# Optimization experiments

Hardware: AMD Instinct MI355X
Metric: run time of the kernel (lower is better)

The kernel has to match this reference:

```python
import jax, jax.numpy as jnp
import numpy as np

B, L, D = 8, 8192, 512


def setup_inputs() -> dict:
    key = jax.random.key(0)
    ks = jax.random.split(key, 8)
    sc = 1.0 / np.sqrt(D).astype(np.float32)
    return {
        "emotion_h": jax.random.normal(ks[0], (B, 1, D), jnp.float32),
        "sents_h": jax.random.normal(ks[1], (B, L, D), jnp.float32),
        "pre_sents_h": jax.random.normal(ks[2], (B, L, D), jnp.float32),
        "pos_sents_h": jax.random.normal(ks[3], (B, L, D), jnp.float32),
        "W1": jax.random.normal(ks[4], (D, D), jnp.float32) * sc,
        "b1": jnp.zeros((D,), jnp.float32),
        "W2": jax.random.normal(ks[5], (D, D), jnp.float32) * sc,
        "b2": jnp.zeros((D,), jnp.float32),
        "W3": jax.random.normal(ks[6], (D, 1), jnp.float32) * sc,
        "b3": jnp.zeros((1,), jnp.float32),
    }


def reference(emotion_h, sents_h, pre_sents_h, pos_sents_h, W1, b1, W2, b2, W3, b3):
    # Attention: score over sentences conditioned on emotion vector.
    eq = emotion_h @ W1 + b1                      # (B, 1, D)
    sq = sents_h @ W2 + b2                        # (B, L, D)
    logits = (jnp.tanh(eq + sq) @ W3 + b3)[..., 0]  # (B, L)
    s = jax.nn.softmax(logits, axis=-1)           # (B, L), sums to 1 over L

    # Original builds (B,L,3,L) tril/eye/triu masks and matmuls with the
    # expanded score -> per-position weights are:
    #   pre_w[i]  = sum_{j<i} s[j]   (tril(-1))
    #   self_w[i] = s[i]             (eye)
    #   pos_w[i]  = sum_{j>i} s[j]   (triu(+1))
    # Equivalent O(L) form via cumsum:
    c = jnp.cumsum(s, axis=-1)                    # inclusive prefix sum
    pre_w = (c - s)[..., None]                    # exclusive prefix sum
    self_w = s[..., None]
    pos_w = (1.0 - c)[..., None]                  # suffix sum (softmax sums to 1)

    # Weighted combine of the three contexts: sum over the 3-context axis.
    return pre_w * pre_sents_h + self_w * sents_h + pos_w * pos_sents_h
```

## Files before the change

kernel.cpp:

```cpp
#include <hip/hip_runtime.h>
#include <hip/hip_bf16.h>

typedef __bf16 v8bf __attribute__((ext_vector_type(8)));
typedef float  v4f  __attribute__((ext_vector_type(4)));

__device__ __forceinline__ float fast_tanh(float x) {
    x = fminf(fmaxf(x, -15.f), 15.f);
    float t = __builtin_amdgcn_exp2f(x * 2.885390081777927f);
    return (t - 1.f) * __builtin_amdgcn_rcpf(t + 1.f);
}

__device__ __forceinline__ v8bf cvt8(float4 f0, float4 f1) {
    v8bf v;
    v[0] = (__bf16)f0.x; v[1] = (__bf16)f0.y; v[2] = (__bf16)f0.z; v[3] = (__bf16)f0.w;
    v[4] = (__bf16)f1.x; v[5] = (__bf16)f1.y; v[6] = (__bf16)f1.z; v[7] = (__bf16)f1.w;
    return v;
}

__global__ __launch_bounds__(256) void k01_prep(const float* __restrict__ W2,
                                                __bf16* __restrict__ w2f,
                                                const float* __restrict__ emo,
                                                const float* __restrict__ W1,
                                                const float* __restrict__ b1,
                                                const float* __restrict__ b2,
                                                float* __restrict__ eqc) {
    if (blockIdx.x < 128) {
        int tid = blockIdx.x * 256 + threadIdx.x;
        int ctg  = tid >> 10;
        int kt   = (tid >> 6) & 15;
        int lane = tid & 63;
        int quad = lane >> 4, col = lane & 15;
        int n = ctg * 16 + col;
        int kbase = kt * 32 + quad * 8;
        v8bf v;
#pragma unroll
        for (int j = 0; j < 8; ++j) v[j] = (__bf16)W2[(kbase + j) * 512 + n];
        *(v8bf*)&w2f[(size_t)tid * 8] = v;
    } else {
        __shared__ float part[4][64];
        int bb = blockIdx.x - 128;
        int b = bb >> 3, d0 = (bb & 7) << 6;
        int t = threadIdx.x;
        int dl = t & 63, ks = t >> 6;
        const float* eb = emo + b * 512;
        float acc = 0.f;
        int kend = ks * 128 + 128;
        for (int k = ks * 128; k < kend; ++k)
            acc += eb[k] * W1[k * 512 + d0 + dl];
        part[ks][dl] = acc;
        __syncthreads();
        if (ks == 0) {
            int d = d0 + dl;
            float r = part[0][dl] + part[1][dl] + part[2][dl] + part[3][dl];
            eqc[b * 512 + d] = r + b1[d] + b2[d];
        }
    }
}

__global__ __launch_bounds__(256, 2) void k2_logits(const float* __restrict__ sents,
                                                    const __bf16* __restrict__ w2f,
                                                    const float* __restrict__ eqc,
                                                    const float* __restrict__ W3,
                                                    float* __restrict__ logits) {
    __shared__ float part[64];
    const int t = threadIdx.x;
    const int row0 = blockIdx.x * 64;
    const int bidx = row0 >> 13;

    const int wave = t >> 6, lane = t & 63;
    const int quad = lane >> 4, lcol = lane & 15;
    const int row_half = wave >> 1, col_half = wave & 1;
    const int rbase_local = row_half * 32;

    v4f acc[8][4];
#pragma unroll
    for (int ct = 0; ct < 8; ++ct)
#pragma unroll
        for (int q = 0; q < 4; ++q) acc[ct][q] = (v4f){0.f, 0.f, 0.f, 0.f};

    const float* a0p = &sents[(size_t)(row0 + rbase_local + lcol) * 512 + quad * 8];
    const float* a1p = a0p + 16 * 512;

#pragma unroll 2
    for (int kt = 0; kt < 16; ++kt) {
        const float4* p0 = (const float4*)(a0p + kt * 32);
        const float4* p1 = (const float4*)(a1p + kt * 32);
        float4 f00 = p0[0], f01 = p0[1];
        float4 f10 = p1[0], f11 = p1[1];
        v8bf a0 = cvt8(f00, f01);
        v8bf a1 = cvt8(f10, f11);
#pragma unroll
        for (int ct = 0; ct < 8; ++ct) {
            const int ctg = (col_half * 8 + ct) * 2;
            const __bf16* bp = &w2f[(size_t)((ctg * 16 + kt) * 64 + lane) * 8];
            v8bf b0 = *(const v8bf*)bp;
            v8bf b1 = *(const v8bf*)(bp + 16 * 64 * 8);
            acc[ct][0] = __builtin_amdgcn_mfma_f32_16x16x32_bf16(a0, b0, acc[ct][0], 0, 0, 0);
            acc[ct][1] = __builtin_amdgcn_mfma_f32_16x16x32_bf16(a0, b1, acc[ct][1], 0, 0, 0);
            acc[ct][2] = __builtin_amdgcn_mfma_f32_16x16x32_bf16(a1, b0, acc[ct][2], 0, 0, 0);
            acc[ct][3] = __builtin_amdgcn_mfma_f32_16x16x32_bf16(a1, b1, acc[ct][3], 0, 0, 0);
        }
    }

    float rowacc[8] = {0.f, 0.f, 0.f, 0.f, 0.f, 0.f, 0.f, 0.f};
#pragma unroll
    for (int ct = 0; ct < 8; ++ct) {
        const int c0 = (col_half * 8 + ct) * 32;
        float e0  = eqc[bidx * 512 + c0 + lcol];
        float e1  = eqc[bidx * 512 + c0 + 16 + lcol];
        float w30 = W3[c0 + lcol];
        float w31 = W3[c0 + 16 + lcol];
#pragma unroll
        for (int i = 0; i < 4; ++i) {
            rowacc[i]     += fast_tanh(e0 + acc[ct][0][i]) * w30
                           + fast_tanh(e1 + acc[ct][1][i]) * w31;
            rowacc[4 + i] += fast_tanh(e0 + acc[ct][2][i]) * w30
                           + fast_tanh(e1 + acc[ct][3][i]) * w31;
        }
    }
#pragma unroll
    for (int off = 1; off < 16; off <<= 1)
#pragma unroll
        for (int i = 0; i < 8; ++i) rowacc[i] += __shfl_xor(rowacc[i], off, 16);

    const int rl = rbase_local + quad * 4;
    if (col_half == 1 && lcol == 0) {
#pragma unroll
        for (int i = 0; i < 4; ++i) {
            part[rl + i]      = rowacc[i];
            part[rl + 16 + i] = rowacc[4 + i];
        }
    }
    __syncthreads();
    if (col_half == 0 && lcol == 0) {
#pragma unroll
        for (int i = 0; i < 4; ++i) {
            logits[row0 + rl + i]      = rowacc[i]     + part[rl + i];
            logits[row0 + rl + 16 + i] = rowacc[4 + i] + part[rl + 16 + i];
        }
    }
}

__global__ __launch_bounds__(1024) void k3_softmax(const float* __restrict__ logits,
                                                   float* __restrict__ sw,
                                                   float* __restrict__ cw) {
    int b = blockIdx.x, t = threadIdx.x;
    const float* lg = logits + b * 8192;
    float v[8];
    float m = -1e30f;
#pragma unroll
    for (int i = 0; i < 8; ++i) { v[i] = lg[t * 8 + i]; m = fmaxf(m, v[i]); }
    __shared__ float red[1024];
    red[t] = m; __syncthreads();
    for (int s = 512; s > 0; s >>= 1) {
        if (t < s) red[t] = fmaxf(red[t], red[t + s]);
        __syncthreads();
    }
    float M = red[0]; __syncthreads();
    float sum = 0.f;
#pragma unroll
    for (int i = 0; i < 8; ++i) {
        v[i] = __builtin_amdgcn_exp2f((v[i] - M) * 1.4426950408889634f);
        sum += v[i];
    }
    red[t] = sum; __syncthreads();
    for (int off = 1; off < 1024; off <<= 1) {
        float add = (t >= off) ? red[t - off] : 0.f;
        __syncthreads();
        red[t] += add;
        __syncthreads();
    }
    float total = red[1023];
    float excl = red[t] - sum;
    float inv = 1.f / total;
    float run = excl;
#pragma unroll
    for (int i = 0; i < 8; ++i) {
        run += v[i];
        sw[b * 8192 + t * 8 + i] = v[i] * inv;
        cw[b * 8192 + t * 8 + i] = run * inv;
    }
}

__global__ __launch_bounds__(256) void k4_combine(const float* __restrict__ sents,
                                                  const float* __restrict__ pre,
                                                  const float* __restrict__ pos,
                                                  const float* __restrict__ sw,
                                                  const float* __restrict__ cw,
                                                  float* __restrict__ out) {
    const size_t stride = (size_t)gridDim.x * 256;
    for (size_t g = (size_t)blockIdx.x * 256 + threadIdx.x; g < 8388608ull; g += stride) {
        size_t base = g << 2;
        int row = (int)(g >> 7);
        float s = sw[row], c = cw[row];
        float pw = c - s, qw = 1.0f - c;
        v4f a = *(const v4f*)&sents[base];
        v4f p = __builtin_nontemporal_load((const v4f*)&pre[base]);
        v4f q = __builtin_nontemporal_load((const v4f*)&pos[base]);
        v4f o = pw * p + s * a + qw * q;
        __builtin_nontemporal_store(o, (v4f*)&out[base]);
    }
}

extern "C" void kernel_launch(void* const* d_in, const int* in_sizes, int n_in,
                              void* d_out, int out_size, void* d_ws, size_t ws_size,
                              hipStream_t stream) {
    const float* emo   = (const float*)d_in[0];
    const float* sents = (const float*)d_in[1];
    const float* pre   = (const float*)d_in[2];
    const float* pos   = (const float*)d_in[3];
    const float* W1    = (const float*)d_in[4];
    const float* b1    = (const float*)d_in[5];
    const float* W2    = (const float*)d_in[6];
    const float* b2    = (const float*)d_in[7];
    const float* W3    = (const float*)d_in[8];
    float* out = (float*)d_out;

    char* ws = (char*)d_ws;
    __bf16* w2f   = (__bf16*)ws;
    float* eqc    = (float*)(ws + 524288);
    float* logits = (float*)(ws + 540672);
    float* sw     = (float*)(ws + 802816);
    float* cw     = (float*)(ws + 1064960);

    k01_prep<<<192, 256, 0, stream>>>(W2, w2f, emo, W1, b1, b2, eqc);
    k2_logits<<<1024, 256, 0, stream>>>(sents, w2f, eqc, W3, logits);
    k3_softmax<<<8, 1024, 0, stream>>>(logits, sw, cw);
    k4_combine<<<2048, 256, 0, stream>>>(sents, pre, pos, sw, cw, out);
}
```

Baseline: 477.3 us.

## Stage sents and W2 tiles in LDS via async global_load_lds double buffering

The logits GEMM kernel now copies each K-slice of the sents rows and of the pre-packed bf16 W2 fragments into shared memory with direct global-to-LDS loads. It double-buffers them so the next slice is fetched while MFMAs run on the current one. Each block now reads W2 once per K-step instead of each wave reading its own slice from global/L2, and the A tile uses an XOR swizzle to avoid LDS bank conflicts. In exchange it uses 80KB of LDS per block, which may limit occupancy, and adds a block barrier every K-step.

Result: faster. 439.7 us (-7.9%).

```diff
diff --git a/kernel.cpp b/kernel.cpp
--- a/kernel.cpp
+++ b/kernel.cpp
@@ -15,6 +15,12 @@
     v[0] = (__bf16)f0.x; v[1] = (__bf16)f0.y; v[2] = (__bf16)f0.z; v[3] = (__bf16)f0.w;
     v[4] = (__bf16)f1.x; v[5] = (__bf16)f1.y; v[6] = (__bf16)f1.z; v[7] = (__bf16)f1.w;
     return v;
+}
+
+__device__ __forceinline__ void gload16(const void* g, void* l) {
+    __builtin_amdgcn_global_load_lds((const __attribute__((address_space(1))) unsigned int*)g,
+                                     (__attribute__((address_space(3))) unsigned int*)l,
+                                     16, 0, 0);
 }
 
 __global__ __launch_bounds__(256) void k01_prep(const float* __restrict__ W2,
@@ -62,7 +68,7 @@
                                                     const float* __restrict__ eqc,
                                                     const float* __restrict__ W3,
                                                     float* __restrict__ logits) {
-    __shared__ float part[64];
+    __shared__ char smem[81920];
     const int t = threadIdx.x;
     const int row0 = blockIdx.x * 64;
     const int bidx = row0 >> 13;
@@ -72,34 +78,65 @@
     const int row_half = wave >> 1, col_half = wave & 1;
     const int rbase_local = row_half * 32;
 
+    const int rA0 = wave * 16 + (lane >> 3);
+    const int rA1 = rA0 + 8;
+    const int sA  = lane & 7;
+    const char* pA0 = (const char*)sents + (size_t)(row0 + rA0) * 2048 + ((sA ^ (rA0 & 7)) << 4);
+    const char* pA1 = (const char*)sents + (size_t)(row0 + rA1) * 2048 + ((sA ^ (rA1 & 7)) << 4);
+    const char* pB = (const char*)w2f + (size_t)wave * 131072 + (lane << 4);
+    char* lA = smem;
+    char* lB = smem + 16384;
+
+    const int r0 = rbase_local + lcol;
+    const int swz = r0 & 7;
+    const int a0c0 = ((2 * quad) ^ swz) << 4;
+    const int a0c1 = ((2 * quad + 1) ^ swz) << 4;
+
     v4f acc[8][4];
 #pragma unroll
     for (int ct = 0; ct < 8; ++ct)
 #pragma unroll
         for (int q = 0; q < 4; ++q) acc[ct][q] = (v4f){0.f, 0.f, 0.f, 0.f};
 
-    const float* a0p = &sents[(size_t)(row0 + rbase_local + lcol) * 512 + quad * 8];
-    const float* a1p = a0p + 16 * 512;
-
-#pragma unroll 2
+    {
+        gload16(pA0, lA + wave * 2048);
+        gload16(pA1, lA + wave * 2048 + 1024);
+#pragma unroll
+        for (int i = 0; i < 8; ++i)
+            gload16(pB + i * 16384, lB + (wave * 8 + i) * 1024);
+    }
+    __syncthreads();
+
+    int cur = 0;
     for (int kt = 0; kt < 16; ++kt) {
-        const float4* p0 = (const float4*)(a0p + kt * 32);
-        const float4* p1 = (const float4*)(a1p + kt * 32);
-        float4 f00 = p0[0], f01 = p0[1];
-        float4 f10 = p1[0], f11 = p1[1];
+        if (kt < 15) {
+            const int nb = cur ^ 1;
+            gload16(pA0 + (kt + 1) * 128, lA + nb * 8192 + wave * 2048);
+            gload16(pA1 + (kt + 1) * 128, lA + nb * 8192 + wave * 2048 + 1024);
+#pragma unroll
+            for (int i = 0; i < 8; ++i)
+                gload16(pB + i * 16384 + (kt + 1) * 1024, lB + nb * 32768 + (wave * 8 + i) * 1024);
+        }
+        const char* aRow0 = lA + cur * 8192 + r0 * 128;
+        const char* bBase = lB + cur * 32768 + (lane << 4);
+        float4 f00 = *(const float4*)(aRow0 + a0c0);
+        float4 f01 = *(const float4*)(aRow0 + a0c1);
+        float4 f10 = *(const float4*)(aRow0 + 16 * 128 + a0c0);
+        float4 f11 = *(const float4*)(aRow0 + 16 * 128 + a0c1);
         v8bf a0 = cvt8(f00, f01);
         v8bf a1 = cvt8(f10, f11);
 #pragma unroll
         for (int ct = 0; ct < 8; ++ct) {
             const int ctg = (col_half * 8 + ct) * 2;
-            const __bf16* bp = &w2f[(size_t)((ctg * 16 + kt) * 64 + lane) * 8];
-            v8bf b0 = *(const v8bf*)bp;
-            v8bf b1 = *(const v8bf*)(bp + 16 * 64 * 8);
+            v8bf b0 = *(const v8bf*)(bBase + ctg * 1024);
+            v8bf b1 = *(const v8bf*)(bBase + (ctg + 1) * 1024);
             acc[ct][0] = __builtin_amdgcn_mfma_f32_16x16x32_bf16(a0, b0, acc[ct][0], 0, 0, 0);
             acc[ct][1] = __builtin_amdgcn_mfma_f32_16x16x32_bf16(a0, b1, acc[ct][1], 0, 0, 0);
             acc[ct][2] = __builtin_amdgcn_mfma_f32_16x16x32_bf16(a1, b0, acc[ct][2], 0, 0, 0);
             acc[ct][3] = __builtin_amdgcn_mfma_f32_16x16x32_bf16(a1, b1, acc[ct][3], 0, 0, 0);
         }
+        __syncthreads();
+        cur ^= 1;
     }
 
     float rowacc[8] = {0.f, 0.f, 0.f, 0.f, 0.f, 0.f, 0.f, 0.f};
@@ -123,6 +160,7 @@
 #pragma unroll
         for (int i = 0; i < 8; ++i) rowacc[i] += __shfl_xor(rowacc[i], off, 16);
 
+    float* part = (float*)smem;
     const int rl = rbase_local + quad * 4;
     if (col_half == 1 && lcol == 0) {
 #pragma unroll
```
